# Kernel optimization log

Measured on AMD Instinct MI355X. Metric: run time of the kernel, lower is better.

The kernel has to match this reference:

```python
import jax, jax.numpy as jnp
import numpy as np

BN_EPS = 1e-5

def setup_inputs() -> dict:
    key = jax.random.key(0)
    ks = jax.random.split(key, 3)
    B, C, H, W = 32, 128, 32, 32
    x = jax.random.normal(ks[0], (B, C, H, W), dtype=jnp.float32)
    w = jax.random.normal(ks[1], (C, C), dtype=jnp.float32) * (1.0 / np.sqrt(C))
    b = jax.random.normal(ks[2], (C,), dtype=jnp.float32) * 0.01
    gamma = jnp.ones((C,), dtype=jnp.float32)
    beta = jnp.zeros((C,), dtype=jnp.float32)
    return {"x": x, "w": w, "b": b, "gamma": gamma, "beta": beta, "k": 9}

def reference(x, w, b, gamma, beta, k):
    B, C, H, W = x.shape
    N = H * W
    tokens = x.reshape(B, C, N).transpose(0, 2, 1)            # (B, N, C)
    # pairwise euclidean distances (torch.cdist, p=2)
    sq = jnp.sum(tokens * tokens, axis=-1)                    # (B, N)
    d2 = sq[:, :, None] + sq[:, None, :] - 2.0 * jnp.einsum('bnc,bmc->bnm', tokens, tokens)
    dist = jnp.sqrt(jnp.maximum(d2, 0.0))                     # (B, N, N)
    # k nearest (smallest distance) neighbors, self included
    _, idx = jax.lax.top_k(-dist, k)                          # idx: (B, N, k)
    gathered = tokens[jnp.arange(B)[:, None, None], idx]      # (B, N, k, C)
    agg = gathered.mean(axis=2)                               # (B, N, C)
    out = jnp.einsum('bnc,dc->bnd', agg, w) + b               # linear
    out = out.transpose(0, 2, 1).reshape(B, C, H, W)
    # BatchNorm2d (training mode: batch stats, biased variance)
    mean = out.mean(axis=(0, 2, 3), keepdims=True)
    var = out.var(axis=(0, 2, 3), keepdims=True)
    bn = gamma[None, :, None, None] * (out - mean) * jax.lax.rsqrt(var + BN_EPS) + beta[None, :, None, None]
    return jax.nn.relu(bn + x)
```

## Files before the change

### kernel.cpp

```cpp
#include <hip/hip_runtime.h>
#include <cfloat>

#define BB 32
#define CH 128
#define NT 1024
#define KNN 9

__global__ __launch_bounds__(256) void k_sq(const float* __restrict__ x,
                                            float* __restrict__ sq,
                                            float* __restrict__ stats) {
  if (blockIdx.x == 0 && blockIdx.y == 0) stats[threadIdx.x] = 0.f;
  const int b = blockIdx.y;
  const int n = blockIdx.x * 256 + threadIdx.x;
  const float* xb = x + (size_t)b * CH * NT + n;
  float s = 0.f;
#pragma unroll 8
  for (int c = 0; c < CH; ++c) {
    float v = xb[(size_t)c * NT];
    s = fmaf(v, v, s);
  }
  sq[b * NT + n] = s;
}

__global__ __launch_bounds__(256) void k_transpose(const float* __restrict__ x,
                                                   float* __restrict__ tok) {
  __shared__ float t[32][33];
  const int b = blockIdx.z, c0 = blockIdx.y * 32, n0 = blockIdx.x * 32;
  const int tx = threadIdx.x, ty = threadIdx.y;
  const float* xb = x + (size_t)b * CH * NT;
#pragma unroll
  for (int k = 0; k < 4; ++k)
    t[ty + 8 * k][tx] = xb[(size_t)(c0 + ty + 8 * k) * NT + n0 + tx];
  __syncthreads();
  float* tb = tok + (size_t)b * NT * CH;
#pragma unroll
  for (int k = 0; k < 4; ++k)
    tb[(size_t)(n0 + ty + 8 * k) * CH + c0 + tx] = t[tx][ty + 8 * k];
}

__global__ __launch_bounds__(256) void k_dist_topk(const float* __restrict__ x,
                                                   const float* __restrict__ sq,
                                                   int* __restrict__ topk) {
  __shared__ float As[32][64];
  __shared__ float Bs[32][128];
  __shared__ float d2s[64][68];
  __shared__ float sqi[64];
  __shared__ float sqj[128];
  const int b = blockIdx.y;
  const int i0 = blockIdx.x * 64;
  const int tid = threadIdx.x;
  const int ty = tid >> 4, tx = tid & 15;
  const float* xb = x + (size_t)b * CH * NT;
  const float* sqb = sq + b * NT;

  if (tid < 64) sqi[tid] = sqb[i0 + tid];

  float val[KNN];
  int idx[KNN];
#pragma unroll
  for (int t = 0; t < KNN; ++t) { val[t] = FLT_MAX; idx[t] = 0x7fffffff; }

  for (int j0 = 0; j0 < NT; j0 += 128) {
    if (tid < 128) sqj[tid] = sqb[j0 + tid];
    float acc[4][8];
#pragma unroll
    for (int r = 0; r < 4; ++r)
#pragma unroll
      for (int q = 0; q < 8; ++q) acc[r][q] = 0.f;

    for (int cc = 0; cc < CH; cc += 32) {
      __syncthreads();
      {
#pragma unroll
        for (int k = 0; k < 2; ++k) {
          int e = tid + k * 256;
          int cl = e >> 4, cf = e & 15;
          *(float4*)&As[cl][cf * 4] =
              *(const float4*)(xb + (size_t)(cc + cl) * NT + i0 + cf * 4);
        }
#pragma unroll
        for (int k = 0; k < 4; ++k) {
          int e = tid + k * 256;
          int cl = e >> 5, cf = e & 31;
          *(float4*)&Bs[cl][cf * 4] =
              *(const float4*)(xb + (size_t)(cc + cl) * NT + j0 + cf * 4);
        }
      }
      __syncthreads();
#pragma unroll
      for (int c = 0; c < 32; ++c) {
        float4 av = *(const float4*)&As[c][ty * 4];
        float4 b0 = *(const float4*)&Bs[c][tx * 4];
        float4 b1 = *(const float4*)&Bs[c][64 + tx * 4];
#define FSTEP(R, AC)                                                        \
  acc[R][0] = fmaf(AC, b0.x, acc[R][0]);                                    \
  acc[R][1] = fmaf(AC, b0.y, acc[R][1]);                                    \
  acc[R][2] = fmaf(AC, b0.z, acc[R][2]);                                    \
  acc[R][3] = fmaf(AC, b0.w, acc[R][3]);                                    \
  acc[R][4] = fmaf(AC, b1.x, acc[R][4]);                                    \
  acc[R][5] = fmaf(AC, b1.y, acc[R][5]);                                    \
  acc[R][6] = fmaf(AC, b1.z, acc[R][6]);                                    \
  acc[R][7] = fmaf(AC, b1.w, acc[R][7]);
        FSTEP(0, av.x) FSTEP(1, av.y) FSTEP(2, av.z) FSTEP(3, av.w)
#undef FSTEP
      }
    }
#pragma unroll
    for (int h = 0; h < 2; ++h) {
#pragma unroll
      for (int r = 0; r < 4; ++r) {
        float si = sqi[ty * 4 + r];
        float4 dv;
        dv.x = sqrtf(fmaxf(si + sqj[h * 64 + tx * 4 + 0] - 2.f * acc[r][4 * h + 0], 0.f));
        dv.y = sqrtf(fmaxf(si + sqj[h * 64 + tx * 4 + 1] - 2.f * acc[r][4 * h + 1], 0.f));
        dv.z = sqrtf(fmaxf(si + sqj[h * 64 + tx * 4 + 2] - 2.f * acc[r][4 * h + 2], 0.f));
        dv.w = sqrtf(fmaxf(si + sqj[h * 64 + tx * 4 + 3] - 2.f * acc[r][4 * h + 3], 0.f));
        *(float4*)&d2s[ty * 4 + r][tx * 4] = dv;
      }
      __syncthreads();
      {
        const int row = tid >> 2, q = tid & 3;
        const int jbase = j0 + h * 64 + q * 16;
        for (int jj = 0; jj < 16; ++jj) {
          float v = d2s[row][q * 16 + jj];
          if (v < val[KNN - 1]) {
            bool gt[KNN];
#pragma unroll
            for (int t = 0; t < KNN; ++t) gt[t] = (val[t] > v);
#pragma unroll
            for (int t = KNN - 1; t >= 1; --t)
              if (gt[t - 1]) { val[t] = val[t - 1]; idx[t] = idx[t - 1]; }
#pragma unroll
            for (int t = 0; t < KNN; ++t)
              if (gt[t] && (t == 0 || !gt[t - 1])) { val[t] = v; idx[t] = jbase + jj; }
          }
        }
      }
      __syncthreads();
    }
  }
  {
    const int base = (tid & 63) & 60;
#pragma unroll
    for (int qq = 1; qq < 4; ++qq) {
#pragma unroll
      for (int t = 0; t < KNN; ++t) {
        float pv = __shfl(val[t], base + qq, 64);
        int pi = __shfl(idx[t], base + qq, 64);
        if ((tid & 3) == 0) {
          bool better = (pv < val[KNN - 1]) ||
                        (pv == val[KNN - 1] && pi < idx[KNN - 1]);
          if (better) {
            bool gt[KNN];
#pragma unroll
            for (int t2 = 0; t2 < KNN; ++t2)
              gt[t2] = (val[t2] > pv) || (val[t2] == pv && idx[t2] > pi);
#pragma unroll
            for (int t2 = KNN - 1; t2 >= 1; --t2)
              if (gt[t2 - 1]) { val[t2] = val[t2 - 1]; idx[t2] = idx[t2 - 1]; }
#pragma unroll
            for (int t2 = 0; t2 < KNN; ++t2)
              if (gt[t2] && (t2 == 0 || !gt[t2 - 1])) { val[t2] = pv; idx[t2] = pi; }
          }
        }
      }
    }
  }
  if ((tid & 3) == 0) {
    const int row = tid >> 2;
    int* tp = topk + ((size_t)b * NT + i0 + row) * KNN;
#pragma unroll
    for (int t = 0; t < KNN; ++t) tp[t] = idx[t];
  }
}

__global__ __launch_bounds__(256) void k_agg_gemm(const float* __restrict__ tok,
                                                  const int* __restrict__ topk,
                                                  const float* __restrict__ w,
                                                  const float* __restrict__ bias,
                                                  float* __restrict__ out) {
  __shared__ float agg_s[64][132];
  __shared__ float w_s[CH][36];
  const int b = blockIdx.y;
  const int n0 = blockIdx.x * 64;
  const int tid = threadIdx.x;
  {
    const int row = tid >> 2, lp = tid & 3;
    const int* tp = topk + ((size_t)b * NT + n0 + row) * KNN;
    float a[32];
#pragma unroll
    for (int i = 0; i < 32; ++i) a[i] = 0.f;
    for (int t = 0; t < KNN; ++t) {
      const float* src = tok + ((size_t)b * NT + tp[t]) * CH + lp * 32;
#pragma unroll
      for (int i = 0; i < 8; ++i) {
        float4 v = *(const float4*)&src[4 * i];
        a[4 * i + 0] += v.x; a[4 * i + 1] += v.y;
        a[4 * i + 2] += v.z; a[4 * i + 3] += v.w;
      }
    }
    const float inv9 = 1.0f / 9.0f;
#pragma unroll
    for (int i = 0; i < 8; ++i) {
      float4 v;
      v.x = a[4 * i + 0] * inv9; v.y = a[4 * i + 1] * inv9;
      v.z = a[4 * i + 2] * inv9; v.w = a[4 * i + 3] * inv9;
      *(float4*)&agg_s[row][lp * 32 + 4 * i] = v;
    }
  }
  const int nn = tid >> 3, dd = tid & 7;
  for (int d0 = 0; d0 < CH; d0 += 32) {
    __syncthreads();
#pragma unroll
    for (int k = 0; k < 16; ++k) {
      int e = tid + k * 256;
      int c = e & 127, dl = e >> 7;
      w_s[c][dl] = w[(size_t)(d0 + dl) * CH + c];
    }
    __syncthreads();
    float acc0[4] = {0.f, 0.f, 0.f, 0.f};
    float acc1[4] = {0.f, 0.f, 0.f, 0.f};
    for (int c4 = 0; c4 < 32; ++c4) {
      float4 a0 = *(const float4*)&agg_s[2 * nn][4 * c4];
      float4 a1 = *(const float4*)&agg_s[2 * nn + 1][4 * c4];
      float4 w0 = *(const float4*)&w_s[4 * c4 + 0][dd * 4];
      float4 w1 = *(const float4*)&w_s[4 * c4 + 1][dd * 4];
      float4 w2 = *(const float4*)&w_s[4 * c4 + 2][dd * 4];
      float4 w3 = *(const float4*)&w_s[4 * c4 + 3][dd * 4];
#define GSTEP(AC, WV)                                                          \
  acc0[0] = fmaf(a0.AC, WV.x, acc0[0]); acc0[1] = fmaf(a0.AC, WV.y, acc0[1]);  \
  acc0[2] = fmaf(a0.AC, WV.z, acc0[2]); acc0[3] = fmaf(a0.AC, WV.w, acc0[3]);  \
  acc1[0] = fmaf(a1.AC, WV.x, acc1[0]); acc1[1] = fmaf(a1.AC, WV.y, acc1[1]);  \
  acc1[2] = fmaf(a1.AC, WV.z, acc1[2]); acc1[3] = fmaf(a1.AC, WV.w, acc1[3]);
      GSTEP(x, w0) GSTEP(y, w1) GSTEP(z, w2) GSTEP(w, w3)
#undef GSTEP
    }
    float* ob = out + ((size_t)b * CH + d0) * NT + n0;
#pragma unroll
    for (int j = 0; j < 4; ++j) {
      float bv = bias[d0 + dd * 4 + j];
      float2 st;
      st.x = acc0[j] + bv;
      st.y = acc1[j] + bv;
      *(float2*)&ob[(size_t)(dd * 4 + j) * NT + 2 * nn] = st;
    }
  }
}

__global__ __launch_bounds__(256) void k_bnstats(const float* __restrict__ out,
                                                 float* __restrict__ stats) {
  const int bc = blockIdx.x;
  const int c = bc & 127;
  const float* p = out + (size_t)bc * NT;
  const int tid = threadIdx.x;
  float4 v = *(const float4*)&p[tid * 4];
  float s = v.x + v.y + v.z + v.w;
  float s2 = v.x * v.x + v.y * v.y + v.z * v.z + v.w * v.w;
#pragma unroll
  for (int o = 32; o > 0; o >>= 1) {
    s += __shfl_down(s, o);
    s2 += __shfl_down(s2, o);
  }
  __shared__ float ls[4], ls2[4];
  const int wid = tid >> 6, lane = tid & 63;
  if (lane == 0) { ls[wid] = s; ls2[wid] = s2; }
  __syncthreads();
  if (tid == 0) {
    atomicAdd(&stats[c], ls[0] + ls[1] + ls[2] + ls[3]);
    atomicAdd(&stats[CH + c], ls2[0] + ls2[1] + ls2[2] + ls2[3]);
  }
}

__global__ __launch_bounds__(256) void k_final(float* out,
                                               const float* __restrict__ x,
                                               const float* __restrict__ gamma,
                                               const float* __restrict__ beta,
                                               const float* __restrict__ stats) {
  const int i = blockIdx.x * 256 + threadIdx.x;
  const int c = (i >> 8) & 127;
  const float m = stats[c] * (1.0f / 32768.0f);
  const float var = stats[CH + c] * (1.0f / 32768.0f) - m * m;
  const float inv = rsqrtf(var + 1e-5f);
  const float g = gamma[c], be = beta[c];
  float4 ov = ((const float4*)out)[i];
  float4 xv = ((const float4*)x)[i];
  float4 r;
  r.x = fmaxf(g * (ov.x - m) * inv + be + xv.x, 0.f);
  r.y = fmaxf(g * (ov.y - m) * inv + be + xv.y, 0.f);
  r.z = fmaxf(g * (ov.z - m) * inv + be + xv.z, 0.f);
  r.w = fmaxf(g * (ov.w - m) * inv + be + xv.w, 0.f);
  ((float4*)out)[i] = r;
}

extern "C" void kernel_launch(void* const* d_in, const int* in_sizes, int n_in,
                              void* d_out, int out_size, void* d_ws, size_t ws_size,
                              hipStream_t stream) {
  const float* x = (const float*)d_in[0];
  const float* w = (const float*)d_in[1];
  const float* bias = (const float*)d_in[2];
  const float* gamma = (const float*)d_in[3];
  const float* beta = (const float*)d_in[4];
  float* out = (float*)d_out;
  char* wsb = (char*)d_ws;
  float* tok = (float*)(wsb);
  float* sq = (float*)(wsb + 16777216);
  int* topk = (int*)(wsb + 16908288);
  float* stats = (float*)(wsb + 18087936);

  k_sq<<<dim3(4, 32), 256, 0, stream>>>(x, sq, stats);
  k_transpose<<<dim3(32, 4, 32), dim3(32, 8), 0, stream>>>(x, tok);
  k_dist_topk<<<dim3(16, 32), 256, 0, stream>>>(x, sq, topk);
  k_agg_gemm<<<dim3(16, 32), 256, 0, stream>>>(tok, topk, w, bias, out);
  k_bnstats<<<4096, 256, 0, stream>>>(out, stats);
  k_final<<<4096, 256, 0, stream>>>(out, x, gamma, beta, stats);
}
```

Measured before the change: 350.6 us.

## Use bf16 MFMA distance pass with candidate top-48 and fp32 rerank

Replaces the fp32 FMA distance GEMM with bf16 MFMA 16x16x32 instructions, reading a bf16 token copy written during the transpose. Selection keeps 12 candidates per lane (48 per row) using packed sort keys built from truncated distance bits plus index, with no sqrt. A new rerank kernel recomputes exact fp32 distances for those 48 candidates and picks the top 9 by wave shuffle reduction. The goal is to cut distance-GEMM and top-k insertion cost. The risks are an extra kernel and workspace traffic, and the approximation being wrong if a true neighbour falls outside the 48 candidates.

```diff
diff --git a/kernel.cpp b/kernel.cpp
--- a/kernel.cpp
+++ b/kernel.cpp
@@ -5,6 +5,18 @@
 #define CH 128
 #define NT 1024
 #define KNN 9
+#define NCAND 48
+
+typedef unsigned int u32;
+typedef unsigned short u16;
+using bf16x8 = __attribute__((ext_vector_type(8))) short;
+using f32x4 = __attribute__((ext_vector_type(4))) float;
+
+__device__ __forceinline__ u16 f2bf(float f) {
+  u32 u = __float_as_uint(f);
+  u32 r = (u + 0x7FFFu + ((u >> 16) & 1u)) >> 16;
+  return (u16)r;
+}
 
 __global__ __launch_bounds__(256) void k_sq(const float* __restrict__ x,
                                             float* __restrict__ sq,
@@ -23,7 +35,8 @@
 }
 
 __global__ __launch_bounds__(256) void k_transpose(const float* __restrict__ x,
-                                                   float* __restrict__ tok) {
+                                                   float* __restrict__ tok,
+                                                   u16* __restrict__ xh) {
   __shared__ float t[32][33];
   const int b = blockIdx.z, c0 = blockIdx.y * 32, n0 = blockIdx.x * 32;
   const int tx = threadIdx.x, ty = threadIdx.y;
@@ -33,144 +46,155 @@
     t[ty + 8 * k][tx] = xb[(size_t)(c0 + ty + 8 * k) * NT + n0 + tx];
   __syncthreads();
   float* tb = tok + (size_t)b * NT * CH;
-#pragma unroll
-  for (int k = 0; k < 4; ++k)
-    tb[(size_t)(n0 + ty + 8 * k) * CH + c0 + tx] = t[tx][ty + 8 * k];
-}
-
-__global__ __launch_bounds__(256) void k_dist_topk(const float* __restrict__ x,
-                                                   const float* __restrict__ sq,
-                                                   int* __restrict__ topk) {
-  __shared__ float As[32][64];
-  __shared__ float Bs[32][128];
-  __shared__ float d2s[64][68];
-  __shared__ float sqi[64];
-  __shared__ float sqj[128];
+  u16* hb = xh + (size_t)b * NT * CH;
+#pragma unroll
+  for (int k = 0; k < 4; ++k) {
+    float v = t[tx][ty + 8 * k];
+    tb[(size_t)(n0 + ty + 8 * k) * CH + c0 + tx] = v;
+    hb[(size_t)(n0 + ty + 8 * k) * CH + c0 + tx] = f2bf(v);
+  }
+}
+
+__global__ __launch_bounds__(256) void k_distf(const u16* __restrict__ xh,
+                                               const float* __restrict__ sq,
+                                               int* __restrict__ cand) {
+  __shared__ float4 Bh4[1024];
+  __shared__ float d2sT[64][68];
+  __shared__ float sqi_s[64];
+  __shared__ float sqj_s[64];
   const int b = blockIdx.y;
   const int i0 = blockIdx.x * 64;
   const int tid = threadIdx.x;
-  const int ty = tid >> 4, tx = tid & 15;
-  const float* xb = x + (size_t)b * CH * NT;
+  const int l = tid & 63, w = tid >> 6;
+  const int l15 = l & 15, lo = l >> 4;
+  const u16* xb = xh + (size_t)b * NT * CH;
   const float* sqb = sq + b * NT;
 
-  if (tid < 64) sqi[tid] = sqb[i0 + tid];
-
-  float val[KNN];
-  int idx[KNN];
-#pragma unroll
-  for (int t = 0; t < KNN; ++t) { val[t] = FLT_MAX; idx[t] = 0x7fffffff; }
-
-  for (int j0 = 0; j0 < NT; j0 += 128) {
-    if (tid < 128) sqj[tid] = sqb[j0 + tid];
-    float acc[4][8];
-#pragma unroll
-    for (int r = 0; r < 4; ++r)
-#pragma unroll
-      for (int q = 0; q < 8; ++q) acc[r][q] = 0.f;
-
-    for (int cc = 0; cc < CH; cc += 32) {
-      __syncthreads();
-      {
-#pragma unroll
-        for (int k = 0; k < 2; ++k) {
-          int e = tid + k * 256;
-          int cl = e >> 4, cf = e & 15;
-          *(float4*)&As[cl][cf * 4] =
-              *(const float4*)(xb + (size_t)(cc + cl) * NT + i0 + cf * 4);
-        }
-#pragma unroll
-        for (int k = 0; k < 4; ++k) {
-          int e = tid + k * 256;
-          int cl = e >> 5, cf = e & 31;
-          *(float4*)&Bs[cl][cf * 4] =
-              *(const float4*)(xb + (size_t)(cc + cl) * NT + j0 + cf * 4);
-        }
+  if (tid < 64) sqi_s[tid] = sqb[i0 + tid];
+
+  bf16x8 af[4];
+#pragma unroll
+  for (int ks = 0; ks < 4; ++ks)
+    af[ks] = *(const bf16x8*)(xb + (size_t)(i0 + 16 * w + l15) * CH + ks * 32 + lo * 8);
+
+  u32 kv[12];
+#pragma unroll
+  for (int t = 0; t < 12; ++t) kv[t] = 0xFFFFFFFFu;
+
+  for (int p = 0; p < 16; ++p) {
+    const int j0 = p * 64;
+    __syncthreads();
+#pragma unroll
+    for (int k = 0; k < 4; ++k) {
+      int e = tid + k * 256;
+      int col = e >> 4, ko = e & 15;
+      u32 byteoff = (u32)(col * 256 + ko * 16) ^ (u32)((col & 7) << 4);
+      Bh4[byteoff >> 4] = *(const float4*)(xb + (size_t)(j0 + col) * CH + ko * 8);
+    }
+    if (tid < 64) sqj_s[tid] = sqb[j0 + tid];
+    __syncthreads();
+    f32x4 acc[4];
+#pragma unroll
+    for (int ct = 0; ct < 4; ++ct) {
+      acc[ct] = (f32x4){0.f, 0.f, 0.f, 0.f};
+#pragma unroll
+      for (int ks = 0; ks < 4; ++ks) {
+        int col = ct * 16 + l15;
+        int ko = ks * 4 + lo;
+        u32 byteoff = (u32)(col * 256 + ko * 16) ^ (u32)((col & 7) << 4);
+        bf16x8 bfr = *(const bf16x8*)((const char*)Bh4 + byteoff);
+        acc[ct] = __builtin_amdgcn_mfma_f32_16x16x32_bf16(af[ks], bfr, acc[ct], 0, 0, 0);
       }
-      __syncthreads();
-#pragma unroll
-      for (int c = 0; c < 32; ++c) {
-        float4 av = *(const float4*)&As[c][ty * 4];
-        float4 b0 = *(const float4*)&Bs[c][tx * 4];
-        float4 b1 = *(const float4*)&Bs[c][64 + tx * 4];
-#define FSTEP(R, AC)                                                        \
-  acc[R][0] = fmaf(AC, b0.x, acc[R][0]);                                    \
-  acc[R][1] = fmaf(AC, b0.y, acc[R][1]);                                    \
-  acc[R][2] = fmaf(AC, b0.z, acc[R][2]);                                    \
-  acc[R][3] = fmaf(AC, b0.w, acc[R][3]);                                    \
-  acc[R][4] = fmaf(AC, b1.x, acc[R][4]);                                    \
-  acc[R][5] = fmaf(AC, b1.y, acc[R][5]);                                    \
-  acc[R][6] = fmaf(AC, b1.z, acc[R][6]);                                    \
-  acc[R][7] = fmaf(AC, b1.w, acc[R][7]);
-        FSTEP(0, av.x) FSTEP(1, av.y) FSTEP(2, av.z) FSTEP(3, av.w)
-#undef FSTEP
-      }
-    }
-#pragma unroll
-    for (int h = 0; h < 2; ++h) {
-#pragma unroll
-      for (int r = 0; r < 4; ++r) {
-        float si = sqi[ty * 4 + r];
-        float4 dv;
-        dv.x = sqrtf(fmaxf(si + sqj[h * 64 + tx * 4 + 0] - 2.f * acc[r][4 * h + 0], 0.f));
-        dv.y = sqrtf(fmaxf(si + sqj[h * 64 + tx * 4 + 1] - 2.f * acc[r][4 * h + 1], 0.f));
-        dv.z = sqrtf(fmaxf(si + sqj[h * 64 + tx * 4 + 2] - 2.f * acc[r][4 * h + 2], 0.f));
-        dv.w = sqrtf(fmaxf(si + sqj[h * 64 + tx * 4 + 3] - 2.f * acc[r][4 * h + 3], 0.f));
-        *(float4*)&d2s[ty * 4 + r][tx * 4] = dv;
-      }
-      __syncthreads();
-      {
-        const int row = tid >> 2, q = tid & 3;
-        const int jbase = j0 + h * 64 + q * 16;
-        for (int jj = 0; jj < 16; ++jj) {
-          float v = d2s[row][q * 16 + jj];
-          if (v < val[KNN - 1]) {
-            bool gt[KNN];
-#pragma unroll
-            for (int t = 0; t < KNN; ++t) gt[t] = (val[t] > v);
-#pragma unroll
-            for (int t = KNN - 1; t >= 1; --t)
-              if (gt[t - 1]) { val[t] = val[t - 1]; idx[t] = idx[t - 1]; }
-#pragma unroll
-            for (int t = 0; t < KNN; ++t)
-              if (gt[t] && (t == 0 || !gt[t - 1])) { val[t] = v; idx[t] = jbase + jj; }
+    }
+    float4 sv = *(const float4*)&sqi_s[16 * w + lo * 4];
+#pragma unroll
+    for (int ct = 0; ct < 4; ++ct) {
+      int col = ct * 16 + l15;
+      float sj = sqj_s[col];
+      float4 dv;
+      dv.x = fmaxf(sv.x + sj - 2.f * acc[ct][0], 0.f);
+      dv.y = fmaxf(sv.y + sj - 2.f * acc[ct][1], 0.f);
+      dv.z = fmaxf(sv.z + sj - 2.f * acc[ct][2], 0.f);
+      dv.w = fmaxf(sv.w + sj - 2.f * acc[ct][3], 0.f);
+      *(float4*)&d2sT[col][16 * w + lo * 4] = dv;
+    }
+    __syncthreads();
+    {
+      const int row = tid >> 2, q = tid & 3;
+#pragma unroll 4
+      for (int jj = 0; jj < 16; ++jj) {
+        int col = q * 16 + jj;
+        float d = d2sT[col][row];
+        u32 key = (__float_as_uint(d) & 0xFFFFFC00u) | (u32)(j0 + col);
+        if (key < kv[11]) {
+          u32 c = key;
+#pragma unroll
+          for (int t = 0; t < 12; ++t) {
+            u32 m = kv[t];
+            kv[t] = m < c ? m : c;
+            c = m < c ? c : m;
           }
         }
       }
-      __syncthreads();
     }
   }
   {
-    const int base = (tid & 63) & 60;
-#pragma unroll
-    for (int qq = 1; qq < 4; ++qq) {
-#pragma unroll
-      for (int t = 0; t < KNN; ++t) {
-        float pv = __shfl(val[t], base + qq, 64);
-        int pi = __shfl(idx[t], base + qq, 64);
-        if ((tid & 3) == 0) {
-          bool better = (pv < val[KNN - 1]) ||
-                        (pv == val[KNN - 1] && pi < idx[KNN - 1]);
-          if (better) {
-            bool gt[KNN];
-#pragma unroll
-            for (int t2 = 0; t2 < KNN; ++t2)
-              gt[t2] = (val[t2] > pv) || (val[t2] == pv && idx[t2] > pi);
-#pragma unroll
-            for (int t2 = KNN - 1; t2 >= 1; --t2)
-              if (gt[t2 - 1]) { val[t2] = val[t2 - 1]; idx[t2] = idx[t2 - 1]; }
-#pragma unroll
-            for (int t2 = 0; t2 < KNN; ++t2)
-              if (gt[t2] && (t2 == 0 || !gt[t2 - 1])) { val[t2] = pv; idx[t2] = pi; }
-          }
-        }
-      }
-    }
-  }
-  if ((tid & 3) == 0) {
-    const int row = tid >> 2;
-    int* tp = topk + ((size_t)b * NT + i0 + row) * KNN;
-#pragma unroll
-    for (int t = 0; t < KNN; ++t) tp[t] = idx[t];
+    const int row = tid >> 2, q = tid & 3;
+    int* cp = cand + ((size_t)b * NT + i0 + row) * NCAND + q * 12;
+#pragma unroll
+    for (int t = 0; t < 12; ++t) cp[t] = (int)(kv[t] & 1023u);
+  }
+}
+
+__global__ __launch_bounds__(256) void k_rerank(const float* __restrict__ tok,
+                                                const float* __restrict__ sq,
+                                                const int* __restrict__ cand,
+                                                int* __restrict__ topk) {
+  const int g = blockIdx.x * 4 + (threadIdx.x >> 6);
+  const int lane = threadIdx.x & 63;
+  const int b = g >> 10, n = g & 1023;
+  const float* trow = tok + (size_t)(b * NT + n) * CH;
+  float v;
+  int ci;
+  if (lane < NCAND) {
+    ci = cand[(size_t)g * NCAND + lane];
+    const float* tc = tok + (size_t)(b * NT + ci) * CH;
+    float acc = 0.f;
+#pragma unroll
+    for (int k = 0; k < 32; ++k) {
+      float4 a = *(const float4*)&trow[4 * k];
+      float4 c4 = *(const float4*)&tc[4 * k];
+      acc = fmaf(a.x, c4.x, acc);
+      acc = fmaf(a.y, c4.y, acc);
+      acc = fmaf(a.z, c4.z, acc);
+      acc = fmaf(a.w, c4.w, acc);
+    }
+    float d2 = sq[b * NT + n] + sq[b * NT + ci] - 2.f * acc;
+    v = sqrtf(fmaxf(d2, 0.f));
+  } else {
+    v = FLT_MAX;
+    ci = 0x7fffffff;
+  }
+  int out[KNN];
+#pragma unroll
+  for (int t = 0; t < KNN; ++t) {
+    float mv = v;
+    int mi = ci;
+#pragma unroll
+    for (int off = 32; off > 0; off >>= 1) {
+      float ov = __shfl_xor(mv, off, 64);
+      int oi = __shfl_xor(mi, off, 64);
+      bool better = (ov < mv) || (ov == mv && oi < mi);
+      mv = better ? ov : mv;
+      mi = better ? oi : mi;
+    }
+    out[t] = mi;
+    if (ci == mi) { v = FLT_MAX; ci = 0x7fffffff; }
+  }
+  if (lane == 0) {
+    int* tp = topk + (size_t)g * KNN;
+#pragma unroll
+    for (int t = 0; t < KNN; ++t) tp[t] = out[t];
   }
 }
 
@@ -303,13 +327,16 @@
   float* out = (float*)d_out;
   char* wsb = (char*)d_ws;
   float* tok = (float*)(wsb);
-  float* sq = (float*)(wsb + 16777216);
-  int* topk = (int*)(wsb + 16908288);
-  float* stats = (float*)(wsb + 18087936);
+  u16* xh = (u16*)(wsb + 16777216);
+  float* sq = (float*)(wsb + 25165824);
+  int* cand = (int*)(wsb + 25296896);
+  int* topk = (int*)(wsb + 31588352);
+  float* stats = (float*)(wsb + 32767744);
 
   k_sq<<<dim3(4, 32), 256, 0, stream>>>(x, sq, stats);
-  k_transpose<<<dim3(32, 4, 32), dim3(32, 8), 0, stream>>>(x, tok);
-  k_dist_topk<<<dim3(16, 32), 256, 0, stream>>>(x, sq, topk);
+  k_transpose<<<dim3(32, 4, 32), dim3(32, 8), 0, stream>>>(x, tok, xh);
+  k_distf<<<dim3(16, 32), 256, 0, stream>>>(xh, sq, cand);
+  k_rerank<<<8192, 256, 0, stream>>>(tok, sq, cand, topk);
   k_agg_gemm<<<dim3(16, 32), 256, 0, stream>>>(tok, topk, w, bias, out);
   k_bnstats<<<4096, 256, 0, stream>>>(out, stats);
   k_final<<<4096, 256, 0, stream>>>(out, x, gamma, beta, stats);
```

Result: no change. 350.5 us (-0.0%).
